# Kernel tuning notes

Hardware: AMD Instinct MI355X
Metric: run time of the kernel (lower is better)

Reference implementation:

```python
import jax, jax.numpy as jnp
import numpy as np

N = 30000      # nodes
E = 480000     # edges
K = 32         # subgraph size per node
P = 16384      # contrastive pairs
IN = 1024      # in_dim
H = 512        # hidden
Z = 128        # latent (zdim)
BN = 8         # batch_num
DB = 16        # dec_batch_dim
DEC0 = Z + DB  # decoder input dim after concat with batch embedding


def _ln(x):
    m = jnp.mean(x, axis=-1, keepdims=True)
    v = jnp.var(x, axis=-1, keepdims=True)
    return (x - m) * jax.lax.rsqrt(v + 1e-5)


def _gin(x, src, dst, W, b, norm=True, act=True):
    # GIN aggregation (eps=0): (1+eps)*x + sum_{j in N(i)} x_j, then MLP/linear
    agg = jax.ops.segment_sum(x[src], dst, num_segments=N)
    h = (x + agg) @ W + b
    if norm:
        h = _ln(h)
    if act:
        h = jax.nn.relu(h)
    return h


def _encode(x, src, dst, W0, b0, W1, b1):
    h = _gin(x, src, dst, W0, b0, norm=True, act=True)
    return _gin(h, src, dst, W1, b1, norm=True, act=True)  # last_norm=True


def _decode(z, src, dst, W0, b0, W1, b1):
    h = _gin(z, src, dst, W0, b0, norm=True, act=True)
    return _gin(h, src, dst, W1, b1, norm=False, act=False)  # last_norm=False


def setup_inputs() -> dict:
    key = jax.random.key(0)
    ks = jax.random.split(key, 24)
    s = 0.02
    inp = {
        "x": jax.random.normal(ks[0], (N, IN), jnp.float32),
        "x_shf": jax.random.normal(ks[1], (N, IN), jnp.float32),
        "batch_labels": jax.random.uniform(ks[2], (N, BN), jnp.float32),
        "enc_W0": s * jax.random.normal(ks[3], (IN, H), jnp.float32),
        "enc_b0": jnp.zeros((H,), jnp.float32),
        "enc_W1": s * jax.random.normal(ks[4], (H, Z), jnp.float32),
        "enc_b1": jnp.zeros((Z,), jnp.float32),
        "dec_W0": s * jax.random.normal(ks[5], (DEC0, H), jnp.float32),
        "dec_b0": jnp.zeros((H,), jnp.float32),
        "dec_W1": s * jax.random.normal(ks[6], (H, IN), jnp.float32),
        "dec_b1": jnp.zeros((IN,), jnp.float32),
        "be_W0": s * jax.random.normal(ks[7], (BN, (BN + DB) // 2), jnp.float32),
        "be_b0": jnp.zeros(((BN + DB) // 2,), jnp.float32),
        "be_W1": s * jax.random.normal(ks[8], ((BN + DB) // 2, DB), jnp.float32),
        "be_b1": jnp.zeros((DB,), jnp.float32),
        "bd_W0": s * jax.random.normal(ks[9], (Z, 64), jnp.float32),
        "bd_b0": jnp.zeros((64,), jnp.float32),
        "bd_W1": s * jax.random.normal(ks[10], (64, BN), jnp.float32),
        "bd_b1": jnp.zeros((BN,), jnp.float32),
        "bil_W": s * jax.random.normal(ks[11], (Z, Z), jnp.float32),
        "edge_index": jax.random.randint(ks[12], (2, E), 0, N, jnp.int32),
        "sub_node_idx": jax.random.randint(ks[13], (N, K), 0, N, jnp.int32),
        "positive_ind": jax.random.randint(ks[14], (P,), 0, N, jnp.int32),
        "negative_ind": jax.random.randint(ks[15], (P,), 0, N, jnp.int32),
    }
    return inp


def reference(x, x_shf, batch_labels, enc_W0, enc_b0, enc_W1, enc_b1,
              dec_W0, dec_b0, dec_W1, dec_b1, be_W0, be_b0, be_W1, be_b1,
              bd_W0, bd_b0, bd_W1, bd_b1, bil_W,
              edge_index, sub_node_idx, positive_ind, negative_ind):
    src, dst = edge_index[0], edge_index[1]

    # encoder + subgraph mean pooling (global_mean_pool over fixed-size subgraphs)
    z_node = _encode(x, src, dst, enc_W0, enc_b0, enc_W1, enc_b1)        # [N, Z]
    z_sub = jnp.mean(z_node[sub_node_idx], axis=1)                        # [N, Z]
    z_node_shf = _encode(x_shf, src, dst, enc_W0, enc_b0, enc_W1, enc_b1)
    z_sub_shf = jnp.mean(z_node_shf[sub_node_idx], axis=1)                # [N, Z]

    # batch encoder (MLP, no norm)
    batch_emb = jax.nn.relu(batch_labels @ be_W0 + be_b0) @ be_W1 + be_b1  # [N, DB]

    # bilinear contrastive discriminator
    zp = z_sub[positive_ind]                                              # [P, Z]
    logits_pos = jnp.einsum('pd,de,pe->p', zp, bil_W, z_sub_shf[positive_ind])
    logits_neg = jnp.einsum('pd,de,pe->p', zp, bil_W, z_sub_shf[negative_ind])

    # batch discriminator (MLP)
    logits_batch = jax.nn.relu(z_sub @ bd_W0 + bd_b0) @ bd_W1 + bd_b1     # [N, BN]

    # decoder over node graph with batch embedding concatenated
    z_node_batch = jnp.concatenate([z_node, batch_emb], axis=1)           # [N, Z+DB]
    recon = _decode(z_node_batch, src, dst, dec_W0, dec_b0, dec_W1, dec_b1)  # [N, IN]

    return (z_sub, z_sub_shf, recon, logits_pos, logits_neg, logits_batch)
```

## Files before the change

### kernel.cpp

```cpp
#include <hip/hip_runtime.h>
#include <hip/hip_bf16.h>

#define N_NODES 30000
#define E_EDGES 480000
#define KSUB 32
#define NPAIR 16384

typedef __hip_bfloat16 bf16;
typedef __bf16 bf16x8 __attribute__((ext_vector_type(8)));
typedef float floatx4 __attribute__((ext_vector_type(4)));

static __device__ __forceinline__ unsigned short f2bu(float f) {
    unsigned int u = __float_as_uint(f);
    unsigned int r = (u + 0x7fffu + ((u >> 16) & 1u)) >> 16;
    return (unsigned short)r;
}
static __device__ __forceinline__ float blo(unsigned int u) { return __uint_as_float(u << 16); }
static __device__ __forceinline__ float bhi(unsigned int u) { return __uint_as_float(u & 0xffff0000u); }
static __device__ __forceinline__ unsigned int pk2(float a, float b) {
    return (unsigned int)f2bu(a) | ((unsigned int)f2bu(b) << 16);
}

__global__ void transpose_pad(const float* __restrict__ W, int K, int Nd,
                              unsigned short* __restrict__ Wt, int Kpad) {
    int t = blockIdx.x * 256 + threadIdx.x;
    if (t >= Nd * Kpad) return;
    int n = t / Kpad, k = t - n * Kpad;
    Wt[t] = (k < K) ? f2bu(W[(size_t)k * Nd + n]) : (unsigned short)0;
}

__global__ void edge_hist(const int* __restrict__ dst, int* __restrict__ deg) {
    int e = blockIdx.x * 256 + threadIdx.x;
    if (e < E_EDGES) atomicAdd(&deg[dst[e]], 1);
}

__global__ void scan_kernel(const int* __restrict__ deg, int N,
                            int* __restrict__ row_start, int* __restrict__ cursor) {
    __shared__ int sh[1024];
    int t = threadIdx.x;
    int chunk = (N + 1023) >> 10;
    int lo = t * chunk;
    int hi = lo + chunk; if (hi > N) hi = N;
    if (lo > N) lo = N;
    int s = 0;
    for (int i = lo; i < hi; i++) s += deg[i];
    sh[t] = s;
    __syncthreads();
    for (int off = 1; off < 1024; off <<= 1) {
        int v = (t >= off) ? sh[t - off] : 0;
        __syncthreads();
        sh[t] += v;
        __syncthreads();
    }
    int run = (t == 0) ? 0 : sh[t - 1];
    for (int i = lo; i < hi; i++) {
        row_start[i] = run; cursor[i] = run; run += deg[i];
    }
    if (t == 1023) row_start[N] = run;
}

__global__ void edge_scatter(const int* __restrict__ src, const int* __restrict__ dst,
                             int* __restrict__ cursor, int* __restrict__ csr_src) {
    int e = blockIdx.x * 256 + threadIdx.x;
    if (e < E_EDGES) {
        int p = atomicAdd(&cursor[dst[e]], 1);
        if (p >= 0 && p < E_EDGES) csr_src[p] = src[e];
    }
}

template <int D, int DOUT, int DO_LN>
__global__ void csr_agg_ln_h(const unsigned short* __restrict__ X,
                             const int* __restrict__ row_start,
                             const int* __restrict__ csr_src,
                             const float* __restrict__ bias,
                             unsigned short* __restrict__ Y,
                             int addCenter, int doRelu) {
    constexpr int VE = (D % 512 == 0) ? 8 : 2;
    constexpr int R = (D + 64 * VE - 1) / (64 * VE);
    static_assert(VE == 2 || R == 1, "VE8 path assumes single round");
    static_assert(!DO_LN || (D % (64 * VE) == 0), "LN path needs full lanes");
    constexpr int U = D / 2;
    constexpr int UO = DOUT / 2;
    static_assert(D % 2 == 0 && DOUT % 2 == 0, "even dims");

    int node = blockIdx.x * 4 + (threadIdx.x >> 6);
    if (node >= N_NODES) return;
    int lane = threadIdx.x & 63;

    float acc[R][VE];
#pragma unroll
    for (int r = 0; r < R; r++)
#pragma unroll
        for (int i = 0; i < VE; i++) acc[r][i] = 0.0f;

    int s0 = row_start[node], s1 = row_start[node + 1];
    if (s0 < 0) s0 = 0;
    if (s1 > E_EDGES) s1 = E_EDGES;

    if constexpr (VE == 8) {
        auto add_u4 = [&](uint4 u) {
            acc[0][0] += blo(u.x); acc[0][1] += bhi(u.x);
            acc[0][2] += blo(u.y); acc[0][3] += bhi(u.y);
            acc[0][4] += blo(u.z); acc[0][5] += bhi(u.z);
            acc[0][6] += blo(u.w); acc[0][7] += bhi(u.w);
        };
        if (addCenter)
            add_u4(*reinterpret_cast<const uint4*>(X + (size_t)node * D + lane * 8));
        for (int j0 = s0; j0 < s1; j0 += 64) {
            int cnt = s1 - j0; if (cnt > 64) cnt = 64;
            int myi = (lane < cnt) ? csr_src[j0 + lane] : 0;
            int t = 0;
            for (; t + 8 <= cnt; t += 8) {
                uint4 raw[8];
#pragma unroll
                for (int g = 0; g < 8; g++) {
                    int s = __shfl(myi, t + g);
                    if ((unsigned)s >= (unsigned)N_NODES) s = 0;
                    raw[g] = *reinterpret_cast<const uint4*>(X + (size_t)s * D + lane * 8);
                }
#pragma unroll
                for (int g = 0; g < 8; g++) add_u4(raw[g]);
            }
            for (; t < cnt; t++) {
                int s = __shfl(myi, t);
                if ((unsigned)s >= (unsigned)N_NODES) s = 0;
                add_u4(*reinterpret_cast<const uint4*>(X + (size_t)s * D + lane * 8));
            }
        }
        if (bias) {
            const float4* bp = reinterpret_cast<const float4*>(bias + lane * 8);
            float4 b0 = bp[0], b1 = bp[1];
            acc[0][0] += b0.x; acc[0][1] += b0.y; acc[0][2] += b0.z; acc[0][3] += b0.w;
            acc[0][4] += b1.x; acc[0][5] += b1.y; acc[0][6] += b1.z; acc[0][7] += b1.w;
        }
    } else {
        auto add_u = [&](int r, unsigned int u) { acc[r][0] += blo(u); acc[r][1] += bhi(u); };
        if (addCenter) {
#pragma unroll
            for (int r = 0; r < R; r++) {
                int unit = r * 64 + lane;
                if (unit < U)
                    add_u(r, *reinterpret_cast<const unsigned int*>(X + (size_t)node * D + unit * 2));
            }
        }
        for (int j0 = s0; j0 < s1; j0 += 64) {
            int cnt = s1 - j0; if (cnt > 64) cnt = 64;
            int myi = (lane < cnt) ? csr_src[j0 + lane] : 0;
            int t = 0;
            for (; t + 8 <= cnt; t += 8) {
                unsigned int raw[8][R];
#pragma unroll
                for (int g = 0; g < 8; g++) {
                    int s = __shfl(myi, t + g);
                    if ((unsigned)s >= (unsigned)N_NODES) s = 0;
#pragma unroll
                    for (int r = 0; r < R; r++) {
                        int unit = r * 64 + lane;
                        raw[g][r] = (unit < U)
                            ? *reinterpret_cast<const unsigned int*>(X + (size_t)s * D + unit * 2)
                            : 0u;
                    }
                }
#pragma unroll
                for (int g = 0; g < 8; g++)
#pragma unroll
                    for (int r = 0; r < R; r++) add_u(r, raw[g][r]);
            }
            for (; t < cnt; t++) {
                int s = __shfl(myi, t);
                if ((unsigned)s >= (unsigned)N_NODES) s = 0;
#pragma unroll
                for (int r = 0; r < R; r++) {
                    int unit = r * 64 + lane;
                    if (unit < U)
                        add_u(r, *reinterpret_cast<const unsigned int*>(X + (size_t)s * D + unit * 2));
                }
            }
        }
        if (bias) {
#pragma unroll
            for (int r = 0; r < R; r++) {
                int unit = r * 64 + lane;
                if (unit < U) { acc[r][0] += bias[unit * 2]; acc[r][1] += bias[unit * 2 + 1]; }
            }
        }
    }

    if constexpr (DO_LN) {
        float s = 0.0f;
#pragma unroll
        for (int r = 0; r < R; r++)
#pragma unroll
            for (int i = 0; i < VE; i++) s += acc[r][i];
        for (int o = 32; o; o >>= 1) s += __shfl_xor(s, o);
        float mean = s * (1.0f / (float)D);
        float q = 0.0f;
#pragma unroll
        for (int r = 0; r < R; r++)
#pragma unroll
            for (int i = 0; i < VE; i++) { float d = acc[r][i] - mean; q += d * d; }
        for (int o = 32; o; o >>= 1) q += __shfl_xor(q, o);
        float rs_ = rsqrtf(q * (1.0f / (float)D) + 1e-5f);
#pragma unroll
        for (int r = 0; r < R; r++)
#pragma unroll
            for (int i = 0; i < VE; i++) acc[r][i] = (acc[r][i] - mean) * rs_;
    }

    if (doRelu) {
#pragma unroll
        for (int r = 0; r < R; r++)
#pragma unroll
            for (int i = 0; i < VE; i++) if (acc[r][i] < 0.0f) acc[r][i] = 0.0f;
    }

    if constexpr (VE == 8) {
        uint4 o = make_uint4(pk2(acc[0][0], acc[0][1]), pk2(acc[0][2], acc[0][3]),
                             pk2(acc[0][4], acc[0][5]), pk2(acc[0][6], acc[0][7]));
        *reinterpret_cast<uint4*>(Y + (size_t)node * DOUT + lane * 8) = o;
    } else {
        constexpr int RO = (UO + 63) / 64;
#pragma unroll
        for (int r = 0; r < RO; r++) {
            int unit = r * 64 + lane;
            if (unit < UO) {
                unsigned int v = 0u;
                if (r < R && unit < U) v = pk2(acc[r][0], acc[r][1]);
                *reinterpret_cast<unsigned int*>(Y + (size_t)node * DOUT + unit * 2) = v;
            }
        }
    }
}

__global__ void ln_relu_h512(const unsigned short* __restrict__ Yin,
                             const float* __restrict__ bias,
                             unsigned short* __restrict__ Out) {
    int row = blockIdx.x * 4 + (threadIdx.x >> 6);
    if (row >= N_NODES) return;
    int lane = threadIdx.x & 63;
    uint4 u = *reinterpret_cast<const uint4*>(Yin + (size_t)row * 512 + lane * 8);
    const float4* bp = reinterpret_cast<const float4*>(bias + lane * 8);
    float4 b0 = bp[0], b1 = bp[1];
    float v[8];
    v[0] = blo(u.x) + b0.x; v[1] = bhi(u.x) + b0.y;
    v[2] = blo(u.y) + b0.z; v[3] = bhi(u.y) + b0.w;
    v[4] = blo(u.z) + b1.x; v[5] = bhi(u.z) + b1.y;
    v[6] = blo(u.w) + b1.z; v[7] = bhi(u.w) + b1.w;
    float s = 0.0f;
#pragma unroll
    for (int i = 0; i < 8; i++) s += v[i];
    for (int o = 32; o; o >>= 1) s += __shfl_xor(s, o);
    float mean = s * (1.0f / 512.0f);
    float q = 0.0f;
#pragma unroll
    for (int i = 0; i < 8; i++) { float d = v[i] - mean; q += d * d; }
    for (int o = 32; o; o >>= 1) q += __shfl_xor(q, o);
    float rs = rsqrtf(q * (1.0f / 512.0f) + 1e-5f);
#pragma unroll
    for (int i = 0; i < 8; i++) {
        float o = (v[i] - mean) * rs;
        v[i] = o > 0.0f ? o : 0.0f;
    }
    uint4 o = make_uint4(pk2(v[0], v[1]), pk2(v[2], v[3]), pk2(v[4], v[5]), pk2(v[6], v[7]));
    *reinterpret_cast<uint4*>(Out + (size_t)row * 512 + lane * 8) = o;
}

template <int ABF, int CBF>
__global__ __launch_bounds__(256, 2) void gemm_bt(
    const void* __restrict__ A_, int lda, const unsigned short* __restrict__ Bt,
    int M, int K, void* __restrict__ C_, int ldc, const float* __restrict__ bias) {
    __shared__ __align__(16) unsigned short As[128 * 72];
    __shared__ __align__(16) unsigned short Bs[128 * 72];
    const int t = threadIdx.x;
    const int lane = t & 63;
    const int wave = t >> 6;
    const int wm = wave >> 1, wn = wave & 1;
    const int quad = lane >> 4, m16 = lane & 15;
    const int bm = blockIdx.x, bn = blockIdx.y;

    floatx4 acc[4][4];
#pragma unroll
    for (int i = 0; i < 4; i++)
#pragma unroll
        for (int j = 0; j < 4; j++)
#pragma unroll
            for (int r = 0; r < 4; r++) acc[i][j][r] = 0.0f;

    union Pk { unsigned short h[8]; uint4 v; };

    for (int k0 = 0; k0 < K; k0 += 64) {
#pragma unroll
        for (int i = 0; i < 4; i++) {
            int q = i * 256 + t;
            int r = q >> 3, g = q & 7;
            int grow = bm * 128 + r;
            uint4 val = make_uint4(0u, 0u, 0u, 0u);
            if (grow < M) {
                if constexpr (ABF) {
                    const unsigned short* Ah = (const unsigned short*)A_;
                    val = *reinterpret_cast<const uint4*>(Ah + (size_t)grow * lda + k0 + g * 8);
                } else {
                    const float* ap = (const float*)A_ + (size_t)grow * lda + k0 + g * 8;
                    float4 f0 = *reinterpret_cast<const float4*>(ap);
                    float4 f1 = *reinterpret_cast<const float4*>(ap + 4);
                    Pk pk;
                    pk.h[0] = f2bu(f0.x); pk.h[1] = f2bu(f0.y);
                    pk.h[2] = f2bu(f0.z); pk.h[3] = f2bu(f0.w);
                    pk.h[4] = f2bu(f1.x); pk.h[5] = f2bu(f1.y);
                    pk.h[6] = f2bu(f1.z); pk.h[7] = f2bu(f1.w);
                    val = pk.v;
                }
            }
            *reinterpret_cast<uint4*>(&As[r * 72 + g * 8]) = val;
        }
#pragma unroll
        for (int i = 0; i < 4; i++) {
            int q = i * 256 + t;
            int r = q >> 3, g = q & 7;
            int grow = bn * 128 + r;
            uint4 val = *reinterpret_cast<const uint4*>(Bt + (size_t)grow * K + k0 + g * 8);
            *reinterpret_cast<uint4*>(&Bs[r * 72 + g * 8]) = val;
        }
        __syncthreads();
#pragma unroll
        for (int kk = 0; kk < 2; kk++) {
            bf16x8 af[4], bfr[4];
#pragma unroll
            for (int i = 0; i < 4; i++) {
                int r = wm * 64 + i * 16 + m16;
                af[i] = *reinterpret_cast<const bf16x8*>(&As[r * 72 + (kk * 4 + quad) * 8]);
            }
#pragma unroll
            for (int j = 0; j < 4; j++) {
                int r = wn * 64 + j * 16 + m16;
                bfr[j] = *reinterpret_cast<const bf16x8*>(&Bs[r * 72 + (kk * 4 + quad) * 8]);
            }
#pragma unroll
            for (int i = 0; i < 4; i++)
#pragma unroll
                for (int j = 0; j < 4; j++)
                    acc[i][j] = __builtin_amdgcn_mfma_f32_16x16x32_bf16(af[i], bfr[j], acc[i][j], 0, 0, 0);
        }
        __syncthreads();
    }
#pragma unroll
    for (int i = 0; i < 4; i++) {
        int r0 = bm * 128 + wm * 64 + i * 16 + quad * 4;
#pragma unroll
        for (int j = 0; j < 4; j++) {
            int c = bn * 128 + wn * 64 + j * 16 + m16;
            float bia = bias ? bias[c] : 0.0f;
#pragma unroll
            for (int r = 0; r < 4; r++) {
                int row = r0 + r;
                if (row < M) {
                    float val = acc[i][j][r] + bia;
                    if constexpr (CBF)
                        ((unsigned short*)C_)[(size_t)row * ldc + c] = f2bu(val);
                    else
                        ((float*)C_)[(size_t)row * ldc + c] = val;
                }
            }
        }
    }
}

__global__ void pool_kernel_h(const unsigned short* __restrict__ zn, const int* __restrict__ idx,
                              float* __restrict__ out) {
    int i = blockIdx.x * 4 + (threadIdx.x >> 6);
    if (i >= N_NODES) return;
    int lane = threadIdx.x & 63;
    int myi = (lane < KSUB) ? idx[i * KSUB + lane] : 0;
    float ax = 0.0f, ay = 0.0f;
#pragma unroll
    for (int t = 0; t < KSUB; t++) {
        int s = __shfl(myi, t);
        if ((unsigned)s >= (unsigned)N_NODES) s = 0;
        unsigned int u = *reinterpret_cast<const unsigned int*>(zn + (size_t)s * 128 + lane * 2);
        ax += blo(u); ay += bhi(u);
    }
    *reinterpret_cast<float2*>(out + (size_t)i * 128 + lane * 2) =
        make_float2(ax * (1.0f / KSUB), ay * (1.0f / KSUB));
}

__global__ void batch_emb_kernel(const float* __restrict__ bl, const float* __restrict__ W0,
                                 const float* __restrict__ b0, const float* __restrict__ W1,
                                 const float* __restrict__ b1, float* __restrict__ out) {
    int i = blockIdx.x * 256 + threadIdx.x;
    if (i >= N_NODES) return;
    float in[8];
#pragma unroll
    for (int d = 0; d < 8; d++) in[d] = bl[(size_t)i * 8 + d];
    float h[12];
#pragma unroll
    for (int j = 0; j < 12; j++) {
        float a = b0[j];
#pragma unroll
        for (int d = 0; d < 8; d++) a += in[d] * W0[d * 12 + j];
        h[j] = a > 0.0f ? a : 0.0f;
    }
#pragma unroll
    for (int j = 0; j < 16; j++) {
        float a = b1[j];
#pragma unroll
        for (int k = 0; k < 12; k++) a += h[k] * W1[k * 16 + j];
        out[(size_t)i * 16 + j] = a;
    }
}

__global__ void concat_kernel_h(const unsigned short* __restrict__ zn,
                                const float* __restrict__ be,
                                unsigned short* __restrict__ znb) {
    int i = blockIdx.x;
    int t = threadIdx.x;
    if (t < 128) znb[(size_t)i * 144 + t] = zn[(size_t)i * 128 + t];
    else if (t < 144) znb[(size_t)i * 144 + t] = f2bu(be[(size_t)i * 16 + (t - 128)]);
}

__global__ void bilinear_dot(const float* __restrict__ U, const float* __restrict__ z_shf,
                             const int* __restrict__ pos, const int* __restrict__ neg,
                             float* __restrict__ out_pos, float* __restrict__ out_neg) {
    int p = blockIdx.x * 4 + (threadIdx.x >> 6);
    if (p >= NPAIR) return;
    int lane = threadIdx.x & 63;
    int ip = pos[p], in_ = neg[p];
    if ((unsigned)ip >= (unsigned)N_NODES) ip = 0;
    if ((unsigned)in_ >= (unsigned)N_NODES) in_ = 0;
    float2 u = *reinterpret_cast<const float2*>(U + (size_t)ip * 128 + lane * 2);
    float2 zp = *reinterpret_cast<const float2*>(z_shf + (size_t)ip * 128 + lane * 2);
    float2 zn = *reinterpret_cast<const float2*>(z_shf + (size_t)in_ * 128 + lane * 2);
    float vp = u.x * zp.x + u.y * zp.y;
    float vn = u.x * zn.x + u.y * zn.y;
    for (int o = 32; o; o >>= 1) { vp += __shfl_xor(vp, o); vn += __shfl_xor(vn, o); }
    if (lane == 0) { out_pos[p] = vp; out_neg[p] = vn; }
}

__global__ void bd_kernel(const float* __restrict__ z_sub, const float* __restrict__ W0,
                          const float* __restrict__ b0, const float* __restrict__ W1,
                          const float* __restrict__ b1, float* __restrict__ out) {
    __shared__ float zsh[4][128];
    __shared__ float hsh[4][64];
    int w = threadIdx.x >> 6, lane = threadIdx.x & 63;
    int node = blockIdx.x * 4 + w;
    zsh[w][lane] = z_sub[(size_t)node * 128 + lane];
    zsh[w][64 + lane] = z_sub[(size_t)node * 128 + 64 + lane];
    __syncthreads();
    float h = b0[lane];
    for (int d = 0; d < 128; d++) h += zsh[w][d] * W0[d * 64 + lane];
    if (h < 0.0f) h = 0.0f;
    hsh[w][lane] = h;
    __syncthreads();
    if (lane < 8) {
        float o = b1[lane];
        for (int l = 0; l < 64; l++) o += hsh[w][l] * W1[l * 8 + lane];
        out[(size_t)node * 8 + lane] = o;
    }
}

extern "C" void kernel_launch(void* const* d_in, const int* in_sizes, int n_in,
                              void* d_out, int out_size, void* d_ws, size_t ws_size,
                              hipStream_t stream) {
    const float* x = (const float*)d_in[0];
    const float* x_shf = (const float*)d_in[1];
    const float* blab = (const float*)d_in[2];
    const float* encW0 = (const float*)d_in[3];
    const float* encb0 = (const float*)d_in[4];
    const float* encW1 = (const float*)d_in[5];
    const float* encb1 = (const float*)d_in[6];
    const float* decW0 = (const float*)d_in[7];
    const float* decb0 = (const float*)d_in[8];
    const float* decW1 = (const float*)d_in[9];
    const float* decb1 = (const float*)d_in[10];
    const float* beW0 = (const float*)d_in[11];
    const float* beb0 = (const float*)d_in[12];
    const float* beW1 = (const float*)d_in[13];
    const float* beb1 = (const float*)d_in[14];
    const float* bdW0 = (const float*)d_in[15];
    const float* bdb0 = (const float*)d_in[16];
    const float* bdW1 = (const float*)d_in[17];
    const float* bdb1 = (const float*)d_in[18];
    const float* bilW = (const float*)d_in[19];
    const int* eidx = (const int*)d_in[20];
    const int* subidx = (const int*)d_in[21];
    const int* posi = (const int*)d_in[22];
    const int* negi = (const int*)d_in[23];
    float* out = (float*)d_out;

    char* ws = (char*)d_ws;
    size_t off = 0;
    auto alloc = [&](size_t bytes) -> void* {
        void* p = ws + off;
        off += (bytes + 255) & ~(size_t)255;
        return p;
    };
    unsigned short* encW0t = (unsigned short*)alloc((size_t)512 * 1024 * 2);
    unsigned short* encW1t = (unsigned short*)alloc((size_t)128 * 512 * 2);
    unsigned short* decW0t = (unsigned short*)alloc((size_t)512 * 192 * 2);
    unsigned short* decW1t = (unsigned short*)alloc((size_t)1024 * 512 * 2);
    unsigned short* bilWt = (unsigned short*)alloc((size_t)128 * 128 * 2);
    int* deg = (int*)alloc((size_t)N_NODES * 4);
    int* row_start = (int*)alloc((size_t)(N_NODES + 1) * 4);
    int* cursor = (int*)alloc((size_t)N_NODES * 4);
    int* csr_src = (int*)alloc((size_t)E_EDGES * 4);
    unsigned short* y0h = (unsigned short*)alloc((size_t)N_NODES * 512 * 2);
    unsigned short* agg0h = (unsigned short*)alloc((size_t)N_NODES * 512 * 2);
    unsigned short* y1h = (unsigned short*)alloc((size_t)N_NODES * 128 * 2);
    unsigned short* znh = (unsigned short*)alloc((size_t)N_NODES * 128 * 2);
    unsigned short* znsh = (unsigned short*)alloc((size_t)N_NODES * 128 * 2);
    unsigned short* znbh = (unsigned short*)alloc((size_t)N_NODES * 144 * 2);
    unsigned short* s1h = (unsigned short*)alloc((size_t)N_NODES * 192 * 2);
    float* bembf = (float*)alloc((size_t)N_NODES * 16 * 4);
    float* Ubil = (float*)alloc((size_t)N_NODES * 128 * 4);
    if (off > ws_size) return;

    const int* e_src = eidx;
    const int* e_dst = eidx + E_EDGES;

    transpose_pad<<<(512 * 1024 + 255) / 256, 256, 0, stream>>>(encW0, 1024, 512, encW0t, 1024);
    transpose_pad<<<(128 * 512 + 255) / 256, 256, 0, stream>>>(encW1, 512, 128, encW1t, 512);
    transpose_pad<<<(512 * 192 + 255) / 256, 256, 0, stream>>>(decW0, 144, 512, decW0t, 192);
    transpose_pad<<<(1024 * 512 + 255) / 256, 256, 0, stream>>>(decW1, 512, 1024, decW1t, 512);
    transpose_pad<<<(128 * 128 + 255) / 256, 256, 0, stream>>>(bilW, 128, 128, bilWt, 128);

    hipMemsetAsync(deg, 0, (size_t)N_NODES * 4, stream);
    edge_hist<<<E_EDGES / 256, 256, 0, stream>>>(e_dst, deg);
    scan_kernel<<<1, 1024, 0, stream>>>(deg, N_NODES, row_start, cursor);
    edge_scatter<<<E_EDGES / 256, 256, 0, stream>>>(e_src, e_dst, cursor, csr_src);

    dim3 gA(235, 4), gB(235, 1), gC(235, 4), gD(235, 8), gU(235, 1);

    for (int pass = 0; pass < 2; pass++) {
        const float* xin = pass ? x_shf : x;
        unsigned short* zn = pass ? znsh : znh;
        float* zsub_out = out + (pass ? 3840000 : 0);
        gemm_bt<0, 1><<<gA, 256, 0, stream>>>(xin, 1024, encW0t, N_NODES, 1024, y0h, 512, nullptr);
        csr_agg_ln_h<512, 512, 1><<<7500, 256, 0, stream>>>(y0h, row_start, csr_src, encb0, agg0h, 1, 1);
        gemm_bt<1, 1><<<gB, 256, 0, stream>>>(agg0h, 512, encW1t, N_NODES, 512, y1h, 128, nullptr);
        csr_agg_ln_h<128, 128, 1><<<7500, 256, 0, stream>>>(y1h, row_start, csr_src, encb1, zn, 1, 1);
        pool_kernel_h<<<7500, 256, 0, stream>>>(zn, subidx, zsub_out);
    }

    batch_emb_kernel<<<(N_NODES + 255) / 256, 256, 0, stream>>>(blab, beW0, beb0, beW1, beb1, bembf);
    concat_kernel_h<<<30000, 192, 0, stream>>>(znh, bembf, znbh);

    csr_agg_ln_h<144, 192, 0><<<7500, 256, 0, stream>>>(znbh, row_start, csr_src, nullptr, s1h, 1, 0);
    gemm_bt<1, 1><<<gC, 256, 0, stream>>>(s1h, 192, decW0t, N_NODES, 192, y0h, 512, nullptr);
    ln_relu_h512<<<7500, 256, 0, stream>>>(y0h, decb0, y0h);
    csr_agg_ln_h<512, 512, 0><<<7500, 256, 0, stream>>>(y0h, row_start, csr_src, nullptr, agg0h, 1, 0);
    gemm_bt<1, 0><<<gD, 256, 0, stream>>>(agg0h, 512, decW1t, N_NODES, 512, out + 7680000, 1024, decb1);

    gemm_bt<0, 0><<<gU, 256, 0, stream>>>(out, 128, bilWt, N_NODES, 128, Ubil, 128, nullptr);
    bilinear_dot<<<(NPAIR + 3) / 4, 256, 0, stream>>>(Ubil, out + 3840000, posi, negi,
                                                      out + 38400000, out + 38416384);
    bd_kernel<<<7500, 256, 0, stream>>>(out, bdW0, bdb0, bdW1, bdb1, out + 38432768);
}
```

Baseline: 1.136 ms.

## Use direct global-to-LDS async loads with XOR swizzle and wider GEMM tiles

The GEMM kernel now loads bf16 tiles straight into LDS with global_load_lds instead of going through registers, and uses an XOR-swizzled 64-wide LDS layout in place of padding to avoid bank conflicts. It is templated on the N tile width: the larger GEMMs use 128x256 tiles with 512 threads, and blocks are remapped to a 1D grid grouped by 8 M-tiles so neighbouring blocks share B and A tiles in cache. The new A-load path drops the row bounds check and relies on an extra workspace allocation to absorb reads past M. LDS use per block grows for the wide tiles, which may limit occupancy.

```diff
diff --git a/kernel.cpp b/kernel.cpp
--- a/kernel.cpp
+++ b/kernel.cpp
@@ -19,6 +19,12 @@
 static __device__ __forceinline__ float bhi(unsigned int u) { return __uint_as_float(u & 0xffff0000u); }
 static __device__ __forceinline__ unsigned int pk2(float a, float b) {
     return (unsigned int)f2bu(a) | ((unsigned int)f2bu(b) << 16);
+}
+
+typedef __attribute__((address_space(1))) const void ga_void;
+typedef __attribute__((address_space(3))) void lds_void;
+static __device__ __forceinline__ void async16(const void* g, void* l) {
+    __builtin_amdgcn_global_load_lds((ga_void*)g, (lds_void*)l, 16, 0, 0);
 }
 
 __global__ void transpose_pad(const float* __restrict__ W, int K, int Nd,
@@ -265,18 +271,31 @@
     *reinterpret_cast<uint4*>(Out + (size_t)row * 512 + lane * 8) = o;
 }
 
-template <int ABF, int CBF>
-__global__ __launch_bounds__(256, 2) void gemm_bt(
+template <int ABF, int CBF, int BLKN>
+__global__ __launch_bounds__(BLKN * 2, 2) void gemm_bt(
     const void* __restrict__ A_, int lda, const unsigned short* __restrict__ Bt,
-    int M, int K, void* __restrict__ C_, int ldc, const float* __restrict__ bias) {
-    __shared__ __align__(16) unsigned short As[128 * 72];
-    __shared__ __align__(16) unsigned short Bs[128 * 72];
+    int M, int K, void* __restrict__ C_, int ldc, const float* __restrict__ bias,
+    int nbn) {
+    constexpr int THREADS = BLKN * 2;
+    constexpr int NW = THREADS / 64;
+    constexpr int WNC = BLKN / 64;
+    constexpr int ASTR = ABF ? 64 : 72;
+    __shared__ __align__(16) unsigned short As[128 * ASTR];
+    __shared__ __align__(16) unsigned short Bs[BLKN * 64];
+
+    int lid = blockIdx.x;
+    int bmlow = lid & 7;
+    int t2 = lid >> 3;
+    int bmh = t2 / nbn;
+    int bn = t2 - bmh * nbn;
+    int bm = bmh * 8 + bmlow;
+    if (bm * 128 >= M) return;
+
     const int t = threadIdx.x;
     const int lane = t & 63;
     const int wave = t >> 6;
-    const int wm = wave >> 1, wn = wave & 1;
+    const int wm = wave / WNC, wn = wave % WNC;
     const int quad = lane >> 4, m16 = lane & 15;
-    const int bm = blockIdx.x, bn = blockIdx.y;
 
     floatx4 acc[4][4];
 #pragma unroll
@@ -287,19 +306,28 @@
             for (int r = 0; r < 4; r++) acc[i][j][r] = 0.0f;
 
     union Pk { unsigned short h[8]; uint4 v; };
+    const int l8 = lane >> 3;
+    const int gseg = (lane & 7) ^ l8;
 
     for (int k0 = 0; k0 < K; k0 += 64) {
-#pragma unroll
-        for (int i = 0; i < 4; i++) {
-            int q = i * 256 + t;
-            int r = q >> 3, g = q & 7;
-            int grow = bm * 128 + r;
-            uint4 val = make_uint4(0u, 0u, 0u, 0u);
-            if (grow < M) {
-                if constexpr (ABF) {
-                    const unsigned short* Ah = (const unsigned short*)A_;
-                    val = *reinterpret_cast<const uint4*>(Ah + (size_t)grow * lda + k0 + g * 8);
-                } else {
+        if constexpr (ABF) {
+            constexpr int ACALLS = 128 / (NW * 8);
+#pragma unroll
+            for (int i = 0; i < ACALLS; i++) {
+                int rb = (i * NW + wave) * 8;
+                const unsigned short* gp = (const unsigned short*)A_ +
+                    (size_t)(bm * 128 + rb + l8) * lda + k0 + gseg * 8;
+                async16(gp, &As[rb * 64]);
+            }
+        } else {
+            constexpr int GR = 1024 / THREADS;
+#pragma unroll
+            for (int i = 0; i < GR; i++) {
+                int q = i * THREADS + t;
+                int r = q >> 3, g = q & 7;
+                int grow = bm * 128 + r;
+                uint4 val = make_uint4(0u, 0u, 0u, 0u);
+                if (grow < M) {
                     const float* ap = (const float*)A_ + (size_t)grow * lda + k0 + g * 8;
                     float4 f0 = *reinterpret_cast<const float4*>(ap);
                     float4 f1 = *reinterpret_cast<const float4*>(ap + 4);
@@ -310,16 +338,15 @@
                     pk.h[6] = f2bu(f1.z); pk.h[7] = f2bu(f1.w);
                     val = pk.v;
                 }
-            }
-            *reinterpret_cast<uint4*>(&As[r * 72 + g * 8]) = val;
-        }
-#pragma unroll
-        for (int i = 0; i < 4; i++) {
-            int q = i * 256 + t;
-            int r = q >> 3, g = q & 7;
-            int grow = bn * 128 + r;
-            uint4 val = *reinterpret_cast<const uint4*>(Bt + (size_t)grow * K + k0 + g * 8);
-            *reinterpret_cast<uint4*>(&Bs[r * 72 + g * 8]) = val;
+                *reinterpret_cast<uint4*>(&As[r * 72 + g * 8]) = val;
+            }
+        }
+        constexpr int BCALLS = BLKN / (NW * 8);
+#pragma unroll
+        for (int i = 0; i < BCALLS; i++) {
+            int rb = (i * NW + wave) * 8;
+            const unsigned short* gp = Bt + (size_t)(bn * BLKN + rb + l8) * K + k0 + gseg * 8;
+            async16(gp, &Bs[rb * 64]);
         }
         __syncthreads();
 #pragma unroll
@@ -328,12 +355,15 @@
 #pragma unroll
             for (int i = 0; i < 4; i++) {
                 int r = wm * 64 + i * 16 + m16;
-                af[i] = *reinterpret_cast<const bf16x8*>(&As[r * 72 + (kk * 4 + quad) * 8]);
+                int off;
+                if constexpr (ABF) off = r * 64 + (((kk * 4 + quad) ^ (r & 7)) * 8);
+                else off = r * 72 + (kk * 4 + quad) * 8;
+                af[i] = *reinterpret_cast<const bf16x8*>(&As[off]);
             }
 #pragma unroll
             for (int j = 0; j < 4; j++) {
                 int r = wn * 64 + j * 16 + m16;
-                bfr[j] = *reinterpret_cast<const bf16x8*>(&Bs[r * 72 + (kk * 4 + quad) * 8]);
+                bfr[j] = *reinterpret_cast<const bf16x8*>(&Bs[r * 64 + (((kk * 4 + quad) ^ (r & 7)) * 8)]);
             }
 #pragma unroll
             for (int i = 0; i < 4; i++)
@@ -348,7 +378,7 @@
         int r0 = bm * 128 + wm * 64 + i * 16 + quad * 4;
 #pragma unroll
         for (int j = 0; j < 4; j++) {
-            int c = bn * 128 + wn * 64 + j * 16 + m16;
+            int c = bn * BLKN + wn * 64 + j * 16 + m16;
             float bia = bias ? bias[c] : 0.0f;
 #pragma unroll
             for (int r = 0; r < 4; r++) {
@@ -511,6 +541,7 @@
     unsigned short* s1h = (unsigned short*)alloc((size_t)N_NODES * 192 * 2);
     float* bembf = (float*)alloc((size_t)N_NODES * 16 * 4);
     float* Ubil = (float*)alloc((size_t)N_NODES * 128 * 4);
+    alloc(262144);
     if (off > ws_size) return;
 
     const int* e_src = eidx;
@@ -527,15 +558,13 @@
     scan_kernel<<<1, 1024, 0, stream>>>(deg, N_NODES, row_start, cursor);
     edge_scatter<<<E_EDGES / 256, 256, 0, stream>>>(e_src, e_dst, cursor, csr_src);
 
-    dim3 gA(235, 4), gB(235, 1), gC(235, 4), gD(235, 8), gU(235, 1);
-
     for (int pass = 0; pass < 2; pass++) {
         const float* xin = pass ? x_shf : x;
         unsigned short* zn = pass ? znsh : znh;
         float* zsub_out = out + (pass ? 3840000 : 0);
-        gemm_bt<0, 1><<<gA, 256, 0, stream>>>(xin, 1024, encW0t, N_NODES, 1024, y0h, 512, nullptr);
+        gemm_bt<0, 1, 256><<<480, 512, 0, stream>>>(xin, 1024, encW0t, N_NODES, 1024, y0h, 512, nullptr, 2);
         csr_agg_ln_h<512, 512, 1><<<7500, 256, 0, stream>>>(y0h, row_start, csr_src, encb0, agg0h, 1, 1);
-        gemm_bt<1, 1><<<gB, 256, 0, stream>>>(agg0h, 512, encW1t, N_NODES, 512, y1h, 128, nullptr);
+        gemm_bt<1, 1, 128><<<240, 256, 0, stream>>>(agg0h, 512, encW1t, N_NODES, 512, y1h, 128, nullptr, 1);
         csr_agg_ln_h<128, 128, 1><<<7500, 256, 0, stream>>>(y1h, row_start, csr_src, encb1, zn, 1, 1);
         pool_kernel_h<<<7500, 256, 0, stream>>>(zn, subidx, zsub_out);
     }
@@ -544,12 +573,12 @@
     concat_kernel_h<<<30000, 192, 0, stream>>>(znh, bembf, znbh);
 
     csr_agg_ln_h<144, 192, 0><<<7500, 256, 0, stream>>>(znbh, row_start, csr_src, nullptr, s1h, 1, 0);
-    gemm_bt<1, 1><<<gC, 256, 0, stream>>>(s1h, 192, decW0t, N_NODES, 192, y0h, 512, nullptr);
+    gemm_bt<1, 1, 256><<<480, 512, 0, stream>>>(s1h, 192, decW0t, N_NODES, 192, y0h, 512, nullptr, 2);
     ln_relu_h512<<<7500, 256, 0, stream>>>(y0h, decb0, y0h);
     csr_agg_ln_h<512, 512, 0><<<7500, 256, 0, stream>>>(y0h, row_start, csr_src, nullptr, agg0h, 1, 0);
-    gemm_bt<1, 0><<<gD, 256, 0, stream>>>(agg0h, 512, decW1t, N_NODES, 512, out + 7680000, 1024, decb1);
-
-    gemm_bt<0, 0><<<gU, 256, 0, stream>>>(out, 128, bilWt, N_NODES, 128, Ubil, 128, nullptr);
+    gemm_bt<1, 0, 256><<<960, 512, 0, stream>>>(agg0h, 512, decW1t, N_NODES, 512, out + 7680000, 1024, decb1, 4);
+
+    gemm_bt<0, 0, 128><<<240, 256, 0, stream>>>(out, 128, bilWt, N_NODES, 128, Ubil, 128, nullptr, 1);
     bilinear_dot<<<(NPAIR + 3) / 4, 256, 0, stream>>>(Ubil, out + 3840000, posi, negi,
                                                       out + 38400000, out + 38416384);
     bd_kernel<<<7500, 256, 0, stream>>>(out, bdW0, bdb0, bdW1, bdb1, out + 38432768);
```

Result: faster. 1.060 ms (-6.7%).
